# Optimization experiments

Measured on AMD Instinct MI355X. Metric: run time of the kernel, lower is better.

## Reference

```python
import jax, jax.numpy as jnp
import numpy as np

N_NODES = 10000
N_EDGES = 160000
BATCH = 32
IN_FEAT = 64
POLY_K = 5
OUT_FEAT = 128


def setup_inputs() -> dict:
    key = jax.random.key(0)
    k_x, k_r, k_c, k_v, k_w, k_b = jax.random.split(key, 6)
    x = jax.random.normal(k_x, (BATCH, N_NODES, IN_FEAT), dtype=jnp.float32)
    lap_rows = jax.random.randint(k_r, (N_EDGES,), 0, N_NODES, dtype=jnp.int32)
    lap_cols = jax.random.randint(k_c, (N_EDGES,), 0, N_NODES, dtype=jnp.int32)
    # small values keep the degree-5 Chebyshev recurrence numerically tame
    lap_vals = jax.random.normal(k_v, (N_EDGES,), dtype=jnp.float32) * 0.05
    weight = jax.random.normal(k_w, (IN_FEAT * POLY_K, OUT_FEAT), dtype=jnp.float32) * 0.1
    bias = jax.random.normal(k_b, (1, 1, OUT_FEAT), dtype=jnp.float32) * 0.1
    return {"x": x, "lap_rows": lap_rows, "lap_cols": lap_cols,
            "lap_vals": lap_vals, "weight": weight, "bias": bias,
            "pooling_size": 4}


def _spmm(rows, cols, vals, m):
    # sparse [N,N] @ dense [N,M] via gather + segment_sum
    return jax.ops.segment_sum(vals[:, None] * m[cols], rows, num_segments=N_NODES)


def reference(x, lap_rows, lap_cols, lap_vals, weight, bias, pooling_size):
    B, N, F = x.shape
    K = POLY_K
    Fo = weight.shape[1]
    # x0: [N, F*B]
    x0 = jnp.transpose(x, (1, 2, 0)).reshape(N, F * B)
    terms = [x0]
    if K > 1:
        x1 = _spmm(lap_rows, lap_cols, lap_vals, x0)
        terms.append(x1)
        for _ in range(2, K):
            x2 = 2.0 * _spmm(lap_rows, lap_cols, lap_vals, x1) - x0
            terms.append(x2)
            x0, x1 = x1, x2
    xk = jnp.stack(terms, axis=0)                      # [K, N, F*B]
    xk = xk.reshape(K, N, F, B)
    xk = jnp.transpose(xk, (3, 1, 2, 0))               # [B, N, F, K]
    xk = xk.reshape(B * N, F * K)
    out = (xk @ weight).reshape(B, N, Fo)              # dense projection
    out = jax.nn.relu(out + bias)                      # bias + ReLU
    if pooling_size > 1:
        out = out.reshape(B, N // pooling_size, pooling_size, Fo).max(axis=2)
    return out
```

## Files before the change

kernel.cpp:

```cpp
#include <hip/hip_runtime.h>
#include <hip/hip_bf16.h>
#include <cstddef>
#include <cstdint>

#define N_NODES 10000
#define N_EDGES 160000
#define BATCH 32
#define IN_FEAT 64
#define POLY_K 5
#define OUT_FEAT 128
#define KTOT 320
#define POOLSZ 4
#define NPOOL 2500
#define NSL 16

typedef short bf16x8 __attribute__((ext_vector_type(8)));
typedef unsigned short u16x8 __attribute__((ext_vector_type(8)));
typedef float f32x4 __attribute__((ext_vector_type(4)));

__device__ __forceinline__ unsigned short f2bf(float f) {
  unsigned int u = __float_as_uint(f);
  unsigned int r = u + 0x7FFFu + ((u >> 16) & 1u);
  return (unsigned short)(r >> 16);
}
__device__ __forceinline__ float bf2f(unsigned short u) {
  return __uint_as_float(((unsigned int)u) << 16);
}


__global__ void zero_int_kernel(int* __restrict__ p, int n) {
  int i = blockIdx.x * 256 + threadIdx.x;
  if (i < n) p[i] = 0;
}

__global__ void hist_kernel(const int* __restrict__ rows, int* __restrict__ deg) {
  int e = blockIdx.x * 256 + threadIdx.x;
  if (e < N_EDGES) atomicAdd(&deg[rows[e]], 1);
}

__global__ void scan_kernel(const int* __restrict__ deg, int* __restrict__ row_start,
                            int* __restrict__ cursor) {
  __shared__ int sm[1024];
  __shared__ int carry;
  int t = threadIdx.x;
  if (t == 0) { carry = 0; row_start[0] = 0; }
  __syncthreads();
  for (int base = 0; base < N_NODES; base += 1024) {
    int idx = base + t;
    int v = (idx < N_NODES) ? deg[idx] : 0;
    sm[t] = v;
    __syncthreads();
    for (int off = 1; off < 1024; off <<= 1) {
      int xv = 0;
      if (t >= off) xv = sm[t - off];
      __syncthreads();
      sm[t] += xv;
      __syncthreads();
    }
    if (idx < N_NODES) {
      int incl = sm[t];
      row_start[idx + 1] = carry + incl;
      cursor[idx] = carry + incl - v;
    }
    __syncthreads();
    if (t == 1023) carry += sm[1023];
    __syncthreads();
  }
}

__global__ void scatter_kernel(const int* __restrict__ rows, const int* __restrict__ cols,
                               const float* __restrict__ vals, int* __restrict__ cursor,
                               int* __restrict__ csr_cols, float* __restrict__ csr_vals) {
  int e = blockIdx.x * 256 + threadIdx.x;
  if (e < N_EDGES) {
    int r = rows[e];
    int p = atomicAdd(&cursor[r], 1);
    csr_cols[p] = cols[e];
    csr_vals[p] = vals[e];
  }
}


__global__ void wpack_kernel(const float* __restrict__ weight, unsigned short* __restrict__ wpack) {
  int id = blockIdx.x * 256 + threadIdx.x;
  if (id >= 5120) return;
  int ft = id / 640;
  int c = (id / 64) % 10;
  int l = id % 64;
  int fo = ft * 16 + (l & 15);
  unsigned short v[8];
  #pragma unroll
  for (int j = 0; j < 8; ++j) {
    int k = c * 32 + ((l >> 4)) * 8 + j;
    int row = (k & 63) * POLY_K + (k >> 6);
    v[j] = f2bf(weight[row * OUT_FEAT + fo]);
  }
  ushort4* dst = (ushort4*)&wpack[(size_t)id * 8];
  dst[0] = make_ushort4(v[0], v[1], v[2], v[3]);
  dst[1] = make_ushort4(v[4], v[5], v[6], v[7]);
}


template <int BB>
__global__ __launch_bounds__(256) void transpose_kernel(const float* __restrict__ x,
                                                        unsigned short* __restrict__ t0, int b0) {
  constexpr int CB = 64 * BB;
  constexpr int SCOLS = CB / NSL;
  constexpr size_t SLICE_SL = (size_t)N_NODES * SCOLS;
  int n = blockIdx.x;
  int t = threadIdx.x;
  for (int i = t * 8; i < CB; i += 2048) {
    int b = i >> 6;
    int f = i & 63;
    const float* xp = &x[((size_t)(b0 + b) * N_NODES + n) * IN_FEAT + f];
    float4 v0 = *(const float4*)xp;
    float4 v1 = *(const float4*)(xp + 4);
    u16x8 o;
    o[0] = f2bf(v0.x); o[1] = f2bf(v0.y); o[2] = f2bf(v0.z); o[3] = f2bf(v0.w);
    o[4] = f2bf(v1.x); o[5] = f2bf(v1.y); o[6] = f2bf(v1.z); o[7] = f2bf(v1.w);
    int sl = i / SCOLS;
    int cw = i & (SCOLS - 1);
    *(u16x8*)&t0[(size_t)sl * SLICE_SL + (size_t)n * SCOLS + cw] = o;
  }
}


template <int BB>
__global__ __launch_bounds__(256) void spmm_kernel(const unsigned short* __restrict__ xin,
                                                   const unsigned short* __restrict__ prev,
                                                   unsigned short* __restrict__ xout,
                                                   const int* __restrict__ row_start,
                                                   const int* __restrict__ csr_cols,
                                                   const float* __restrict__ csr_vals,
                                                   float alpha, int use_prev) {
  constexpr int CB = 64 * BB;
  constexpr int SCOLS = CB / NSL;
  constexpr size_t SLICE_SL = (size_t)N_NODES * SCOLS;
  constexpr int LPR = SCOLS / 8;
  constexpr int RPB = 256 / LPR;
  constexpr int RB = (N_NODES + RPB - 1) / RPB;
  constexpr int PHB = RB * 8;
  int bid = blockIdx.x;
  int phase = bid / PHB;
  int rem = bid - phase * PHB;
  int xcd = rem & 7;
  int rowblk = rem >> 3;
  int slice = phase * 8 + xcd;
  int t = threadIdx.x;
  int rl = t / LPR;
  int cl = t - rl * LPR;
  int n = rowblk * RPB + rl;
  if (n >= N_NODES) return;
  int off = cl * 8;

  const unsigned short* xs = xin  + (size_t)slice * SLICE_SL;
  const unsigned short* ps = prev + (size_t)slice * SLICE_SL;
  unsigned short*       os = xout + (size_t)slice * SLICE_SL;

  int s = row_start[n];
  int e = row_start[n + 1];
  float acc[8];
  #pragma unroll
  for (int j = 0; j < 8; ++j) acc[j] = 0.f;

  int i = s;
  for (; i + 3 < e; i += 4) {
    int c0 = csr_cols[i + 0], c1 = csr_cols[i + 1];
    int c2 = csr_cols[i + 2], c3 = csr_cols[i + 3];
    float v0 = csr_vals[i + 0], v1 = csr_vals[i + 1];
    float v2 = csr_vals[i + 2], v3 = csr_vals[i + 3];
    u16x8 p0 = *(const u16x8*)&xs[(size_t)c0 * SCOLS + off];
    u16x8 p1 = *(const u16x8*)&xs[(size_t)c1 * SCOLS + off];
    u16x8 p2 = *(const u16x8*)&xs[(size_t)c2 * SCOLS + off];
    u16x8 p3 = *(const u16x8*)&xs[(size_t)c3 * SCOLS + off];
    #pragma unroll
    for (int j = 0; j < 8; ++j) {
      acc[j] = fmaf(v0, bf2f(p0[j]), acc[j]);
      acc[j] = fmaf(v1, bf2f(p1[j]), acc[j]);
      acc[j] = fmaf(v2, bf2f(p2[j]), acc[j]);
      acc[j] = fmaf(v3, bf2f(p3[j]), acc[j]);
    }
  }
  for (; i < e; ++i) {
    int c0 = csr_cols[i];
    float v0 = csr_vals[i];
    u16x8 p0 = *(const u16x8*)&xs[(size_t)c0 * SCOLS + off];
    #pragma unroll
    for (int j = 0; j < 8; ++j) acc[j] = fmaf(v0, bf2f(p0[j]), acc[j]);
  }

  u16x8 o;
  if (use_prev) {
    u16x8 q = *(const u16x8*)&ps[(size_t)n * SCOLS + off];
    #pragma unroll
    for (int j = 0; j < 8; ++j) o[j] = f2bf(alpha * acc[j] - bf2f(q[j]));
  } else {
    #pragma unroll
    for (int j = 0; j < 8; ++j) o[j] = f2bf(alpha * acc[j]);
  }
  *(u16x8*)&os[(size_t)n * SCOLS + off] = o;
}


template <int BB>
__global__ __launch_bounds__(256, 4) void gemm_mfma_kernel(const unsigned short* __restrict__ slices,
                                                           const unsigned short* __restrict__ wpack,
                                                           const float* __restrict__ bias,
                                                           float* __restrict__ out, int b0) {
  constexpr int CB = 64 * BB;
  constexpr int SCOLS = CB / NSL;
  constexpr size_t SLICE_SL = (size_t)N_NODES * SCOLS;
  constexpr int MB = (BB >= 16) ? 16 : BB;
  constexpr int MT = MB / 4;
  constexpr int SPAN = MB * 64;
  constexpr int ROWS = 4 * MB;
  __shared__ unsigned short A[ROWS * 320];

  int g = blockIdx.x;
  int bh = blockIdx.y;
  int t = threadIdx.x;

  constexpr int CHUNKS = ROWS * 40;
  for (int idx0 = 0; idx0 < CHUNKS; idx0 += 256) {
    int idx = idx0 + t;
    int row = idx / 40;
    int cphys = idx - row * 40;
    int clog = cphys ^ (row & 7);
    int kpoly = clog >> 3;
    int fb = (clog & 7) * 8;
    int bloc = row >> 2;
    int nd = row & 3;
    int c = bh * SPAN + bloc * 64 + fb;
    int sl = c / SCOLS;
    int cw = c & (SCOLS - 1);
    const unsigned short* gsrc = &slices[((size_t)kpoly * NSL + sl) * SLICE_SL +
                                         (size_t)(g * POOLSZ + nd) * SCOLS + cw];
    unsigned short* lbase = &A[(size_t)(idx0 + (t & 192)) * 8];
    __builtin_amdgcn_global_load_lds((const __attribute__((address_space(1))) unsigned int*)gsrc,
                                     (__attribute__((address_space(3))) unsigned int*)lbase,
                                     16, 0, 0);
  }
  __syncthreads();

  int w = t >> 6;
  int l = t & 63;
  int lm = l & 15;
  int q = l >> 4;
  int swz = lm & 7;

  f32x4 acc[MT][2];
  #pragma unroll
  for (int mt = 0; mt < MT; ++mt)
    #pragma unroll
    for (int fj = 0; fj < 2; ++fj) {
      acc[mt][fj][0] = 0.f; acc[mt][fj][1] = 0.f;
      acc[mt][fj][2] = 0.f; acc[mt][fj][3] = 0.f;
    }

  #pragma unroll
  for (int c = 0; c < 10; ++c) {
    bf16x8 bfrag[2];
    #pragma unroll
    for (int fj = 0; fj < 2; ++fj) {
      int fi = w * 2 + fj;
      bfrag[fj] = *(const bf16x8*)&wpack[(size_t)(((fi * 10) + c) * 64 + l) * 8];
    }
    #pragma unroll
    for (int mt = 0; mt < MT; ++mt) {
      bf16x8 afrag = *(const bf16x8*)&A[(mt * 16 + lm) * 320 + (((c * 4 + q) ^ swz) << 3)];
      acc[mt][0] = __builtin_amdgcn_mfma_f32_16x16x32_bf16(afrag, bfrag[0], acc[mt][0], 0, 0, 0);
      acc[mt][1] = __builtin_amdgcn_mfma_f32_16x16x32_bf16(afrag, bfrag[1], acc[mt][1], 0, 0, 0);
    }
  }

  #pragma unroll
  for (int fj = 0; fj < 2; ++fj) {
    int fo = (w * 2 + fj) * 16 + lm;
    float bv = bias[fo];
    #pragma unroll
    for (int mt = 0; mt < MT; ++mt) {
      float mx = fmaxf(fmaxf(acc[mt][fj][0], acc[mt][fj][1]),
                       fmaxf(acc[mt][fj][2], acc[mt][fj][3]));
      float val = fmaxf(mx + bv, 0.f);
      int b = b0 + bh * MB + mt * 4 + q;
      out[((size_t)b * NPOOL + g) * OUT_FEAT + fo] = val;
    }
  }
}


template <int BB>
static void run_pipeline(const float* x, const float* bias,
                         const int* row_start, const int* csr_cols, const float* csr_vals,
                         const unsigned short* wpack,
                         unsigned short* slices, float* out, hipStream_t stream) {
  constexpr int CB = 64 * BB;
  constexpr size_t TERM = (size_t)N_NODES * CB;
  constexpr int LPR = (CB / NSL) / 8;
  constexpr int RPB = 256 / LPR;
  constexpr int NBLK = ((N_NODES + RPB - 1) / RPB) * NSL;
  constexpr int MB = (BB >= 16) ? 16 : BB;
  for (int b0 = 0; b0 < BATCH; b0 += BB) {
    transpose_kernel<BB><<<N_NODES, 256, 0, stream>>>(x, slices, b0);
    for (int k = 1; k < POLY_K; ++k) {
      const unsigned short* xin  = slices + (size_t)(k - 1) * TERM;
      const unsigned short* prev = (k >= 2) ? slices + (size_t)(k - 2) * TERM : slices;
      unsigned short* xout = slices + (size_t)k * TERM;
      float alpha = (k == 1) ? 1.0f : 2.0f;
      spmm_kernel<BB><<<NBLK, 256, 0, stream>>>(xin, prev, xout, row_start,
                                                csr_cols, csr_vals, alpha,
                                                (k >= 2) ? 1 : 0);
    }
    gemm_mfma_kernel<BB><<<dim3(NPOOL, BB / MB), 256, 0, stream>>>(slices, wpack, bias, out, b0);
  }
}

static size_t needed_bytes(int BB) {
  return 1482112u + (size_t)6400000 * BB;
}

extern "C" void kernel_launch(void* const* d_in, const int* in_sizes, int n_in,
                              void* d_out, int out_size, void* d_ws, size_t ws_size,
                              hipStream_t stream) {
  const float* x        = (const float*)d_in[0];
  const int*   lap_rows = (const int*)d_in[1];
  const int*   lap_cols = (const int*)d_in[2];
  const float* lap_vals = (const float*)d_in[3];
  const float* weight   = (const float*)d_in[4];
  const float* bias     = (const float*)d_in[5];
  float* out = (float*)d_out;

  int* deg       = (int*)d_ws;
  int* cursor    = deg + 10016;
  int* row_start = cursor + 10016;
  int* csr_cols  = row_start + 10016;
  float* csr_vals = (float*)(csr_cols + N_EDGES);
  unsigned short* wpack = (unsigned short*)(csr_vals + N_EDGES);
  unsigned short* slices = wpack + 40960;

  int BB = 0;
  if      (ws_size >= needed_bytes(32)) BB = 32;
  else if (ws_size >= needed_bytes(16)) BB = 16;
  else if (ws_size >= needed_bytes(8))  BB = 8;
  else if (ws_size >= needed_bytes(4))  BB = 4;
  if (BB == 0) return;

  zero_int_kernel<<<(N_NODES + 255) / 256, 256, 0, stream>>>(deg, N_NODES);
  hist_kernel<<<(N_EDGES + 255) / 256, 256, 0, stream>>>(lap_rows, deg);
  scan_kernel<<<1, 1024, 0, stream>>>(deg, row_start, cursor);
  scatter_kernel<<<(N_EDGES + 255) / 256, 256, 0, stream>>>(lap_rows, lap_cols, lap_vals,
                                                            cursor, csr_cols, csr_vals);
  wpack_kernel<<<20, 256, 0, stream>>>(weight, wpack);

  switch (BB) {
    case 32: run_pipeline<32>(x, bias, row_start, csr_cols, csr_vals, wpack, slices, out, stream); break;
    case 16: run_pipeline<16>(x, bias, row_start, csr_cols, csr_vals, wpack, slices, out, stream); break;
    case 8:  run_pipeline<8>(x, bias, row_start, csr_cols, csr_vals, wpack, slices, out, stream); break;
    case 4:  run_pipeline<4>(x, bias, row_start, csr_cols, csr_vals, wpack, slices, out, stream); break;
  }
}
```

Before: 444.1 us.

## Sort SpMM rows by degree and use packed bf16 unpack with 2-wide FMAs

Adds a degree histogram, scan and counting-sort pass that builds a permutation of nodes ordered by degree, reusing the cursor buffer. The SpMM kernel then processes rows in that order, so lanes in a wavefront have similar neighbour counts and less divergence. The inner loop now loads 32-bit pairs, unpacks two bf16 values at once and accumulates with 2-wide vector FMAs, and uses 32-bit index arithmetic. This costs three extra small preprocessing launches and destroys spatial locality of output writes.

```diff
diff --git a/kernel.cpp b/kernel.cpp
--- a/kernel.cpp
+++ b/kernel.cpp
@@ -16,7 +16,9 @@
 
 typedef short bf16x8 __attribute__((ext_vector_type(8)));
 typedef unsigned short u16x8 __attribute__((ext_vector_type(8)));
+typedef unsigned int u32x4 __attribute__((ext_vector_type(4)));
 typedef float f32x4 __attribute__((ext_vector_type(4)));
+typedef float f32x2 __attribute__((ext_vector_type(2)));
 
 __device__ __forceinline__ unsigned short f2bf(float f) {
   unsigned int u = __float_as_uint(f);
@@ -25,6 +27,12 @@
 }
 __device__ __forceinline__ float bf2f(unsigned short u) {
   return __uint_as_float(((unsigned int)u) << 16);
+}
+__device__ __forceinline__ f32x2 unpk(unsigned int u) {
+  f32x2 r;
+  r[0] = __uint_as_float(u << 16);
+  r[1] = __uint_as_float(u & 0xFFFF0000u);
+  return r;
 }
 
 
@@ -77,6 +85,40 @@
     int p = atomicAdd(&cursor[r], 1);
     csr_cols[p] = cols[e];
     csr_vals[p] = vals[e];
+  }
+}
+
+
+__global__ void dhist_kernel(const int* __restrict__ deg, int* __restrict__ dhist) {
+  int i = blockIdx.x * 256 + threadIdx.x;
+  if (i < N_NODES) {
+    int d = deg[i]; if (d > 255) d = 255;
+    atomicAdd(&dhist[d], 1);
+  }
+}
+
+__global__ void dscan_kernel(const int* __restrict__ dhist, int* __restrict__ dcur) {
+  __shared__ int sm[256];
+  int t = threadIdx.x;
+  int v = dhist[t];
+  sm[t] = v;
+  __syncthreads();
+  for (int off = 1; off < 256; off <<= 1) {
+    int x = (t >= off) ? sm[t - off] : 0;
+    __syncthreads();
+    sm[t] += x;
+    __syncthreads();
+  }
+  dcur[t] = sm[t] - v;
+}
+
+__global__ void psort_kernel(const int* __restrict__ deg, int* __restrict__ dcur,
+                             int* __restrict__ perm) {
+  int i = blockIdx.x * 256 + threadIdx.x;
+  if (i < N_NODES) {
+    int d = deg[i]; if (d > 255) d = 255;
+    int p = atomicAdd(&dcur[d], 1);
+    perm[p] = i;
   }
 }
 
@@ -132,6 +174,7 @@
                                                    const int* __restrict__ row_start,
                                                    const int* __restrict__ csr_cols,
                                                    const float* __restrict__ csr_vals,
+                                                   const int* __restrict__ perm,
                                                    float alpha, int use_prev) {
   constexpr int CB = 64 * BB;
   constexpr int SCOLS = CB / NSL;
@@ -149,9 +192,10 @@
   int t = threadIdx.x;
   int rl = t / LPR;
   int cl = t - rl * LPR;
-  int n = rowblk * RPB + rl;
-  if (n >= N_NODES) return;
-  int off = cl * 8;
+  int si = rowblk * RPB + rl;
+  if (si >= N_NODES) return;
+  int n = perm[si];
+  unsigned off = (unsigned)cl * 8u;
 
   const unsigned short* xs = xin  + (size_t)slice * SLICE_SL;
   const unsigned short* ps = prev + (size_t)slice * SLICE_SL;
@@ -159,9 +203,7 @@
 
   int s = row_start[n];
   int e = row_start[n + 1];
-  float acc[8];
-  #pragma unroll
-  for (int j = 0; j < 8; ++j) acc[j] = 0.f;
+  f32x2 a0 = {0.f, 0.f}, a1 = {0.f, 0.f}, a2 = {0.f, 0.f}, a3 = {0.f, 0.f};
 
   int i = s;
   for (; i + 3 < e; i += 4) {
@@ -169,36 +211,55 @@
     int c2 = csr_cols[i + 2], c3 = csr_cols[i + 3];
     float v0 = csr_vals[i + 0], v1 = csr_vals[i + 1];
     float v2 = csr_vals[i + 2], v3 = csr_vals[i + 3];
-    u16x8 p0 = *(const u16x8*)&xs[(size_t)c0 * SCOLS + off];
-    u16x8 p1 = *(const u16x8*)&xs[(size_t)c1 * SCOLS + off];
-    u16x8 p2 = *(const u16x8*)&xs[(size_t)c2 * SCOLS + off];
-    u16x8 p3 = *(const u16x8*)&xs[(size_t)c3 * SCOLS + off];
-    #pragma unroll
-    for (int j = 0; j < 8; ++j) {
-      acc[j] = fmaf(v0, bf2f(p0[j]), acc[j]);
-      acc[j] = fmaf(v1, bf2f(p1[j]), acc[j]);
-      acc[j] = fmaf(v2, bf2f(p2[j]), acc[j]);
-      acc[j] = fmaf(v3, bf2f(p3[j]), acc[j]);
-    }
+    u32x4 d0 = *(const u32x4*)&xs[(unsigned)c0 * SCOLS + off];
+    u32x4 d1 = *(const u32x4*)&xs[(unsigned)c1 * SCOLS + off];
+    u32x4 d2 = *(const u32x4*)&xs[(unsigned)c2 * SCOLS + off];
+    u32x4 d3 = *(const u32x4*)&xs[(unsigned)c3 * SCOLS + off];
+    f32x2 w0 = {v0, v0}, w1 = {v1, v1}, w2 = {v2, v2}, w3 = {v3, v3};
+    a0 = __builtin_elementwise_fma(w0, unpk(d0[0]), a0);
+    a1 = __builtin_elementwise_fma(w0, unpk(d0[1]), a1);
+    a2 = __builtin_elementwise_fma(w0, unpk(d0[2]), a2);
+    a3 = __builtin_elementwise_fma(w0, unpk(d0[3]), a3);
+    a0 = __builtin_elementwise_fma(w1, unpk(d1[0]), a0);
+    a1 = __builtin_elementwise_fma(w1, unpk(d1[1]), a1);
+    a2 = __builtin_elementwise_fma(w1, unpk(d1[2]), a2);
+    a3 = __builtin_elementwise_fma(w1, unpk(d1[3]), a3);
+    a0 = __builtin_elementwise_fma(w2, unpk(d2[0]), a0);
+    a1 = __builtin_elementwise_fma(w2, unpk(d2[1]), a1);
+    a2 = __builtin_elementwise_fma(w2, unpk(d2[2]), a2);
+    a3 = __builtin_elementwise_fma(w2, unpk(d2[3]), a3);
+    a0 = __builtin_elementwise_fma(w3, unpk(d3[0]), a0);
+    a1 = __builtin_elementwise_fma(w3, unpk(d3[1]), a1);
+    a2 = __builtin_elementwise_fma(w3, unpk(d3[2]), a2);
+    a3 = __builtin_elementwise_fma(w3, unpk(d3[3]), a3);
   }
   for (; i < e; ++i) {
     int c0 = csr_cols[i];
     float v0 = csr_vals[i];
-    u16x8 p0 = *(const u16x8*)&xs[(size_t)c0 * SCOLS + off];
-    #pragma unroll
-    for (int j = 0; j < 8; ++j) acc[j] = fmaf(v0, bf2f(p0[j]), acc[j]);
-  }
-
+    u32x4 d0 = *(const u32x4*)&xs[(unsigned)c0 * SCOLS + off];
+    f32x2 w0 = {v0, v0};
+    a0 = __builtin_elementwise_fma(w0, unpk(d0[0]), a0);
+    a1 = __builtin_elementwise_fma(w0, unpk(d0[1]), a1);
+    a2 = __builtin_elementwise_fma(w0, unpk(d0[2]), a2);
+    a3 = __builtin_elementwise_fma(w0, unpk(d0[3]), a3);
+  }
+
+  unsigned nelt = (unsigned)n * SCOLS + off;
   u16x8 o;
   if (use_prev) {
-    u16x8 q = *(const u16x8*)&ps[(size_t)n * SCOLS + off];
-    #pragma unroll
-    for (int j = 0; j < 8; ++j) o[j] = f2bf(alpha * acc[j] - bf2f(q[j]));
+    u32x4 qd = *(const u32x4*)&ps[nelt];
+    f32x2 q0 = unpk(qd[0]), q1 = unpk(qd[1]), q2 = unpk(qd[2]), q3 = unpk(qd[3]);
+    o[0] = f2bf(alpha * a0[0] - q0[0]); o[1] = f2bf(alpha * a0[1] - q0[1]);
+    o[2] = f2bf(alpha * a1[0] - q1[0]); o[3] = f2bf(alpha * a1[1] - q1[1]);
+    o[4] = f2bf(alpha * a2[0] - q2[0]); o[5] = f2bf(alpha * a2[1] - q2[1]);
+    o[6] = f2bf(alpha * a3[0] - q3[0]); o[7] = f2bf(alpha * a3[1] - q3[1]);
   } else {
-    #pragma unroll
-    for (int j = 0; j < 8; ++j) o[j] = f2bf(alpha * acc[j]);
-  }
-  *(u16x8*)&os[(size_t)n * SCOLS + off] = o;
+    o[0] = f2bf(alpha * a0[0]); o[1] = f2bf(alpha * a0[1]);
+    o[2] = f2bf(alpha * a1[0]); o[3] = f2bf(alpha * a1[1]);
+    o[4] = f2bf(alpha * a2[0]); o[5] = f2bf(alpha * a2[1]);
+    o[6] = f2bf(alpha * a3[0]); o[7] = f2bf(alpha * a3[1]);
+  }
+  *(u16x8*)&os[nelt] = o;
 }
 
 
@@ -292,7 +353,7 @@
 template <int BB>
 static void run_pipeline(const float* x, const float* bias,
                          const int* row_start, const int* csr_cols, const float* csr_vals,
-                         const unsigned short* wpack,
+                         const int* perm, const unsigned short* wpack,
                          unsigned short* slices, float* out, hipStream_t stream) {
   constexpr int CB = 64 * BB;
   constexpr size_t TERM = (size_t)N_NODES * CB;
@@ -308,7 +369,7 @@
       unsigned short* xout = slices + (size_t)k * TERM;
       float alpha = (k == 1) ? 1.0f : 2.0f;
       spmm_kernel<BB><<<NBLK, 256, 0, stream>>>(xin, prev, xout, row_start,
-                                                csr_cols, csr_vals, alpha,
+                                                csr_cols, csr_vals, perm, alpha,
                                                 (k >= 2) ? 1 : 0);
     }
     gemm_mfma_kernel<BB><<<dim3(NPOOL, BB / MB), 256, 0, stream>>>(slices, wpack, bias, out, b0);
@@ -316,7 +377,7 @@
 }
 
 static size_t needed_bytes(int BB) {
-  return 1482112u + (size_t)6400000 * BB;
+  return 1484160u + (size_t)6400000 * BB;
 }
 
 extern "C" void kernel_launch(void* const* d_in, const int* in_sizes, int n_in,
@@ -333,7 +394,9 @@
   int* deg       = (int*)d_ws;
   int* cursor    = deg + 10016;
   int* row_start = cursor + 10016;
-  int* csr_cols  = row_start + 10016;
+  int* dhist     = row_start + 10016;
+  int* dcur      = dhist + 256;
+  int* csr_cols  = dcur + 256;
   float* csr_vals = (float*)(csr_cols + N_EDGES);
   unsigned short* wpack = (unsigned short*)(csr_vals + N_EDGES);
   unsigned short* slices = wpack + 40960;
@@ -346,16 +409,20 @@
   if (BB == 0) return;
 
   zero_int_kernel<<<(N_NODES + 255) / 256, 256, 0, stream>>>(deg, N_NODES);
+  zero_int_kernel<<<2, 256, 0, stream>>>(dhist, 512);
   hist_kernel<<<(N_EDGES + 255) / 256, 256, 0, stream>>>(lap_rows, deg);
   scan_kernel<<<1, 1024, 0, stream>>>(deg, row_start, cursor);
   scatter_kernel<<<(N_EDGES + 255) / 256, 256, 0, stream>>>(lap_rows, lap_cols, lap_vals,
                                                             cursor, csr_cols, csr_vals);
+  dhist_kernel<<<(N_NODES + 255) / 256, 256, 0, stream>>>(deg, dhist);
+  dscan_kernel<<<1, 256, 0, stream>>>(dhist, dcur);
+  psort_kernel<<<(N_NODES + 255) / 256, 256, 0, stream>>>(deg, dcur, cursor);
   wpack_kernel<<<20, 256, 0, stream>>>(weight, wpack);
 
   switch (BB) {
-    case 32: run_pipeline<32>(x, bias, row_start, csr_cols, csr_vals, wpack, slices, out, stream); break;
-    case 16: run_pipeline<16>(x, bias, row_start, csr_cols, csr_vals, wpack, slices, out, stream); break;
-    case 8:  run_pipeline<8>(x, bias, row_start, csr_cols, csr_vals, wpack, slices, out, stream); break;
-    case 4:  run_pipeline<4>(x, bias, row_start, csr_cols, csr_vals, wpack, slices, out, stream); break;
-  }
-}
+    case 32: run_pipeline<32>(x, bias, row_start, csr_cols, csr_vals, cursor, wpack, slices, out, stream); break;
+    case 16: run_pipeline<16>(x, bias, row_start, csr_cols, csr_vals, cursor, wpack, slices, out, stream); break;
+    case 8:  run_pipeline<8>(x, bias, row_start, csr_cols, csr_vals, cursor, wpack, slices, out, stream); break;
+    case 4:  run_pipeline<4>(x, bias, row_start, csr_cols, csr_vals, cursor, wpack, slices, out, stream); break;
+  }
+}
```

After: 498.2 us. 1.12x slower.
